# Kernel tuning notes

Hardware: AMD Instinct MI355X
Metric: run time of the kernel (lower is better)

Reference implementation:

```python
import jax, jax.numpy as jnp
import numpy as np

BS, NUM_PATCH, N_VARS, PATCH_LEN, D_MODEL = 32, 64, 321, 12, 128
TIME_RATIO, FREQ_RATIO = 0.5, 0.4


def setup_inputs() -> dict:
    key = jax.random.key(0)
    ks = jax.random.split(key, 7)
    x = jax.random.normal(ks[0], (BS, NUM_PATCH, N_VARS, PATCH_LEN), jnp.float32)
    W_in = jax.random.normal(ks[1], (PATCH_LEN, D_MODEL), jnp.float32) / np.sqrt(PATCH_LEN)
    b_in = jnp.zeros((D_MODEL,), jnp.float32)
    W_out = jax.random.normal(ks[2], (D_MODEL, PATCH_LEN), jnp.float32) / np.sqrt(D_MODEL)
    b_out = jnp.zeros((PATCH_LEN,), jnp.float32)
    # nn.Parameter(torch.zeros(1,1,1)) in the original; use small random scalars so grads are non-trivial
    time_mask_token = jax.random.normal(ks[3], (), jnp.float32) * 0.02
    freq_mask_token = jax.random.normal(ks[4], (), jnp.float32) * 0.02
    return {"x": x, "W_in": W_in, "b_in": b_in, "W_out": W_out, "b_out": b_out,
            "time_mask_token": time_mask_token, "freq_mask_token": freq_mask_token}


def _scatter_mask(idx, num_patch):
    # idx: [bs, n_vars, k] patch indices to mask (set False). Returns bool [bs, num_patch, n_vars].
    bs, nv, k = idx.shape
    m = jnp.ones((bs, num_patch, nv), dtype=bool)
    b = jnp.arange(bs)[:, None, None]
    v = jnp.arange(nv)[None, :, None]
    return m.at[b, idx, v].set(False)


def reference(x, W_in, b_in, W_out, b_out, time_mask_token, freq_mask_token):
    bs, num_patch, n_vars, patch_len = x.shape

    # patch2emb applied per token (equivalent to the gather-encode path since the
    # projection is pointwise per patch): [bs, np, nv, d_model]
    emb = jnp.einsum('bpvl,ld->bpvd', x, W_in) + b_in

    # ---- time masking: mask patches with highest coefficient of variation ----
    cv = jnp.std(x, axis=-1, ddof=1) / (jnp.mean(x, axis=-1) + 1e-6)  # [bs, np, nv]
    k_t = int(num_patch * TIME_RATIO)
    _, idx_t = jax.lax.top_k(jnp.transpose(cv, (0, 2, 1)), k_t)       # [bs, nv, k_t]
    mask_t = _scatter_mask(idx_t, num_patch)                           # True = keep
    tokens_t = jnp.where(mask_t[..., None], emb, time_mask_token)
    out_t = jnp.einsum('bpvd,dl->bpvl', tokens_t, W_out) + b_out

    # ---- freq masking: mask patches with lowest mean FFT magnitude ----
    mag = jnp.abs(jnp.fft.rfft(x, axis=-1))                            # [bs, np, nv, pl//2+1]
    score = mag.mean(axis=-1)                                          # [bs, np, nv]
    k_f = int(num_patch * FREQ_RATIO)
    _, idx_f = jax.lax.top_k(-jnp.transpose(score, (0, 2, 1)), k_f)    # smallest scores
    mask_f = _scatter_mask(idx_f, num_patch)
    tokens_f = jnp.where(mask_f[..., None], emb, freq_mask_token)
    out_f = jnp.einsum('bpvd,dl->bpvl', tokens_f, W_out) + b_out

    return out_t * 0.5 + out_f * 0.5
```

## Files before the change

### kernel.cpp

```cpp
#include <hip/hip_runtime.h>
#include <math.h>

constexpr int BS = 32, NP = 64, NV = 321, PL = 12, DM = 128;
constexpr int KT = 32;
constexpr int KF = 25;

__global__ void prep_kernel(const float* __restrict__ W_in,
                            const float* __restrict__ b_in,
                            const float* __restrict__ W_out,
                            const float* __restrict__ tt,
                            const float* __restrict__ ft,
                            float* __restrict__ prep) {
  int t = threadIdx.x;
  if (t < 144) {
    int i = t / 12, l = t % 12;
    float s = 0.f;
    for (int d = 0; d < DM; ++d) s += W_in[i * DM + d] * W_out[d * PL + l];
    prep[t] = s;
  } else if (t < 156) {
    int l = t - 144;
    float cs = 0.f, cb = 0.f;
    for (int d = 0; d < DM; ++d) {
      float w = W_out[d * PL + l];
      cs += w;
      cb += b_in[d] * w;
    }
    prep[144 + l] = cb;
    prep[156 + l] = tt[0] * cs;
    prep[168 + l] = ft[0] * cs;
  }
}

__global__ __launch_bounds__(256) void score_mask_kernel(
    const float* __restrict__ x,
    unsigned long long* __restrict__ mT,
    unsigned long long* __restrict__ mF) {
  const int wave = threadIdx.x >> 6;
  const int p = threadIdx.x & 63;
  const int bv = blockIdx.x * 4 + wave;
  const int b = bv / NV, v = bv % NV;

  const float4* xp = (const float4*)(x + ((size_t)(b * NP + p) * NV + v) * PL);
  float4 a0 = xp[0], a1 = xp[1], a2 = xp[2];
  float xv[12] = {a0.x, a0.y, a0.z, a0.w, a1.x, a1.y, a1.z, a1.w,
                  a2.x, a2.y, a2.z, a2.w};

  float s = 0.f;
#pragma unroll
  for (int i = 0; i < 12; ++i) s += xv[i];
  float m = s * (1.0f / 12.0f);
  float ss = 0.f;
#pragma unroll
  for (int i = 0; i < 12; ++i) {
    float d = xv[i] - m;
    ss += d * d;
  }
  float cv = sqrtf(ss * (1.0f / 11.0f)) / (m + 1e-6f);

  const float C30[12] = {1.f, 0.86602540378443864676f, 0.5f, 0.f,
                         -0.5f, -0.86602540378443864676f, -1.f,
                         -0.86602540378443864676f, -0.5f, 0.f,
                         0.5f, 0.86602540378443864676f};
  const float S30[12] = {0.f, 0.5f, 0.86602540378443864676f, 1.f,
                         0.86602540378443864676f, 0.5f, 0.f,
                         -0.5f, -0.86602540378443864676f, -1.f,
                         -0.86602540378443864676f, -0.5f};
  float acc = 0.f;
#pragma unroll
  for (int k = 0; k < 7; ++k) {
    float re = 0.f, im = 0.f;
#pragma unroll
    for (int n = 0; n < 12; ++n) {
      int idx = (k * n) % 12;
      re += xv[n] * C30[idx];
      im += xv[n] * S30[idx];
    }
    acc += sqrtf(re * re + im * im);
  }
  float fs = acc * (1.0f / 7.0f);

  __shared__ float scv[4][64];
  __shared__ float sfs[4][64];
  scv[wave][p] = cv;
  sfs[wave][p] = fs;
  __syncthreads();
  int rt = 0, rf = 0;
#pragma unroll 4
  for (int q = 0; q < 64; ++q) {
    float cq = scv[wave][q];
    rt += (cq > cv || (cq == cv && q < p)) ? 1 : 0;
    float fq = sfs[wave][q];
    rf += (fq < fs || (fq == fs && q < p)) ? 1 : 0;
  }
  bool keep_t = (rt >= KT);
  bool keep_f = (rf >= KF);
  unsigned long long bt = __ballot(keep_t);
  unsigned long long bf = __ballot(keep_f);
  if (p == 0) {
    mT[bv] = bt;
    mF[bv] = bf;
  }
}

__global__ __launch_bounds__(256) void decode_kernel(
    const float* __restrict__ x,
    const float* __restrict__ b_out,
    const float* __restrict__ prep,
    const unsigned long long* __restrict__ mT,
    const unsigned long long* __restrict__ mF,
    float* __restrict__ out) {
  const int bp = blockIdx.x;
  const int b = bp >> 6, p = bp & 63;
  __shared__ float sM[144], sc[12], sSt[12], sSf[12], sb[12];
  __shared__ float xs[NV * PL];
  const int tid = threadIdx.x;
  if (tid < 144) sM[tid] = prep[tid];
  else if (tid < 156) sc[tid - 144] = prep[tid];
  else if (tid < 168) sSt[tid - 156] = prep[tid];
  else if (tid < 180) sSf[tid - 168] = prep[tid];
  else if (tid < 192) sb[tid - 180] = b_out[tid - 180];

  const float4* xbp = (const float4*)(x + (size_t)bp * (NV * PL));
  float4* xs4 = (float4*)xs;
  for (int i = tid; i < NV * PL / 4; i += 256) xs4[i] = xbp[i];
  __syncthreads();

  float* outp = out + (size_t)bp * (NV * PL);
  for (int e = tid; e < NV * PL; e += 256) {
    int v = e / 12, l = e - v * 12;
    float E = sc[l];
#pragma unroll
    for (int i = 0; i < 12; ++i) E += xs[v * 12 + i] * sM[i * 12 + l];
    unsigned long long mt = mT[b * NV + v];
    unsigned long long mf = mF[b * NV + v];
    bool kt = (mt >> p) & 1ull;
    bool kf = (mf >> p) & 1ull;
    float at = kt ? E : sSt[l];
    float af = kf ? E : sSf[l];
    outp[e] = 0.5f * (at + af) + sb[l];
  }
}

extern "C" void kernel_launch(void* const* d_in, const int* in_sizes, int n_in,
                              void* d_out, int out_size, void* d_ws,
                              size_t ws_size, hipStream_t stream) {
  const float* x = (const float*)d_in[0];
  const float* W_in = (const float*)d_in[1];
  const float* b_in = (const float*)d_in[2];
  const float* W_out = (const float*)d_in[3];
  const float* b_out = (const float*)d_in[4];
  const float* tt = (const float*)d_in[5];
  const float* ft = (const float*)d_in[6];
  float* out = (float*)d_out;

  float* prep = (float*)d_ws;
  unsigned long long* mT = (unsigned long long*)((char*)d_ws + 1024);
  unsigned long long* mF = mT + BS * NV;

  hipLaunchKernelGGL(prep_kernel, dim3(1), dim3(192), 0, stream, W_in, b_in,
                     W_out, tt, ft, prep);
  hipLaunchKernelGGL(score_mask_kernel, dim3(BS * NV / 4), dim3(256), 0,
                     stream, x, mT, mF);
  hipLaunchKernelGGL(decode_kernel, dim3(BS * NP), dim3(256), 0, stream, x,
                     b_out, prep, mT, mF, out);
}
```

Baseline: 129.1 us.

## Fuse prep, scoring/masking and decode into one kernel with ballot-based top-k

Replaces three launches with a single fused kernel. Each block loads an 8-variable strip of x for all 64 patches into padded shared memory, recomputes the small weight product per block, scores patches and builds the masks, then decodes and writes float4 outputs. The O(64) rank loop is replaced by a wave-wide radix select over ordered float bits using ballots, and the 12-point DFT uses a symmetric closed form. This removes the second read of x and the launch overhead, at the cost of recomputing W_in·W_out in every block and using strided x loads.

```diff
diff --git a/kernel.cpp b/kernel.cpp
--- a/kernel.cpp
+++ b/kernel.cpp
@@ -4,140 +4,214 @@
 constexpr int BS = 32, NP = 64, NV = 321, PL = 12, DM = 128;
 constexpr int KT = 32;
 constexpr int KF = 25;
-
-__global__ void prep_kernel(const float* __restrict__ W_in,
-                            const float* __restrict__ b_in,
-                            const float* __restrict__ W_out,
-                            const float* __restrict__ tt,
-                            const float* __restrict__ ft,
-                            float* __restrict__ prep) {
-  int t = threadIdx.x;
+constexpr int VB = 8;
+constexpr int NCHUNK = (NV + VB - 1) / VB;
+constexpr int RSTRIDE = 64 * 13 + 4;
+
+__device__ __forceinline__ unsigned ord(float f) {
+  unsigned u = __float_as_uint(f);
+  return ((int)u < 0) ? ~u : (u | 0x80000000u);
+}
+
+__device__ __forceinline__ bool keep_not_topk(unsigned u, int K, int lane) {
+  unsigned thr = 0;
+#pragma unroll
+  for (int bit = 31; bit >= 0; --bit) {
+    unsigned cand = thr | (1u << bit);
+    unsigned long long b = __ballot(u >= cand);
+    if (__popcll(b) >= K) thr = cand;
+  }
+  int cnt_gt = __popcll(__ballot(u > thr));
+  unsigned long long eq = __ballot(u == thr);
+  int r_eq = __popcll(eq & ((1ull << lane) - 1ull));
+  bool masked = (u > thr) || ((u == thr) && (r_eq < (K - cnt_gt)));
+  return !masked;
+}
+
+__global__ __launch_bounds__(256) void fused_kernel(
+    const float* __restrict__ x, const float* __restrict__ W_in,
+    const float* __restrict__ b_in, const float* __restrict__ W_out,
+    const float* __restrict__ b_out, const float* __restrict__ tt,
+    const float* __restrict__ ft, float* __restrict__ out) {
+  __shared__ float xs[VB * RSTRIDE];
+  __shared__ float sM[144];
+  __shared__ float sc[12], sSt[12], sSf[12], sb[12];
+  __shared__ unsigned long long smT[VB], smF[VB];
+
+  const int t = threadIdx.x;
+  const int blk = blockIdx.x;
+  const int b = blk / NCHUNK;
+  const int chunk = blk - b * NCHUNK;
+  const int v0 = chunk * VB;
+  const int nv = min(VB, NV - v0);
+
+  const float* xb = x + (size_t)(b * 64) * (NV * PL) + v0 * PL;
+  const int nf4 = 64 * nv * 3;
+  float4 st[6];
+  int soff[6];
+  int cnt = 0;
+  for (int j = t; j < nf4; j += 256) {
+    int p = j / (nv * 3);
+    int r = j - p * (nv * 3);
+    int vv = r / 3;
+    int l0 = (r - vv * 3) * 4;
+    st[cnt] = *(const float4*)(xb + (size_t)p * (NV * PL) + vv * PL + l0);
+    soff[cnt] = vv * RSTRIDE + p * 13 + l0;
+    ++cnt;
+  }
+
   if (t < 144) {
-    int i = t / 12, l = t % 12;
-    float s = 0.f;
-    for (int d = 0; d < DM; ++d) s += W_in[i * DM + d] * W_out[d * PL + l];
-    prep[t] = s;
-  } else if (t < 156) {
-    int l = t - 144;
+    const int i = t / 12, l = t - (t / 12) * 12;
+    const float4* Wi = (const float4*)(W_in + i * DM);
+    float acc = 0.f;
+#pragma unroll 8
+    for (int d4 = 0; d4 < 32; ++d4) {
+      float4 a = Wi[d4];
+      const float* wo = W_out + d4 * 48 + l;
+      acc += a.x * wo[0];
+      acc += a.y * wo[12];
+      acc += a.z * wo[24];
+      acc += a.w * wo[36];
+    }
+    sM[t] = acc;
+  } else if (t < 168) {
+    const int l = (t - 144) % 12;
     float cs = 0.f, cb = 0.f;
+#pragma unroll 8
     for (int d = 0; d < DM; ++d) {
-      float w = W_out[d * PL + l];
+      float w = W_out[d * 12 + l];
       cs += w;
       cb += b_in[d] * w;
     }
-    prep[144 + l] = cb;
-    prep[156 + l] = tt[0] * cs;
-    prep[168 + l] = ft[0] * cs;
-  }
-}
-
-__global__ __launch_bounds__(256) void score_mask_kernel(
-    const float* __restrict__ x,
-    unsigned long long* __restrict__ mT,
-    unsigned long long* __restrict__ mF) {
-  const int wave = threadIdx.x >> 6;
-  const int p = threadIdx.x & 63;
-  const int bv = blockIdx.x * 4 + wave;
-  const int b = bv / NV, v = bv % NV;
-
-  const float4* xp = (const float4*)(x + ((size_t)(b * NP + p) * NV + v) * PL);
-  float4 a0 = xp[0], a1 = xp[1], a2 = xp[2];
-  float xv[12] = {a0.x, a0.y, a0.z, a0.w, a1.x, a1.y, a1.z, a1.w,
-                  a2.x, a2.y, a2.z, a2.w};
-
-  float s = 0.f;
-#pragma unroll
-  for (int i = 0; i < 12; ++i) s += xv[i];
-  float m = s * (1.0f / 12.0f);
-  float ss = 0.f;
+    if (t < 156) {
+      sc[l] = cb;
+      sSt[l] = tt[0] * cs;
+    } else {
+      sSf[l] = ft[0] * cs;
+    }
+  } else if (t < 180) {
+    sb[t - 168] = b_out[t - 168];
+  }
+
+  for (int q = 0; q < cnt; ++q) {
+    float* d = xs + soff[q];
+    d[0] = st[q].x;
+    d[1] = st[q].y;
+    d[2] = st[q].z;
+    d[3] = st[q].w;
+  }
+  __syncthreads();
+
+  const int wv = t >> 6, lane = t & 63;
+  const float H = 0.86602540378443864676f;
+#pragma unroll
+  for (int k = 0; k < 2; ++k) {
+    const int vv = wv * 2 + k;
+    if (vv < nv) {
+      const float* xp = xs + vv * RSTRIDE + lane * 13;
+      float xv[12];
+#pragma unroll
+      for (int i = 0; i < 12; ++i) xv[i] = xp[i];
+
+      float s = 0.f;
+#pragma unroll
+      for (int i = 0; i < 12; ++i) s += xv[i];
+      const float m = s * (1.0f / 12.0f);
+      float ss = 0.f;
+#pragma unroll
+      for (int i = 0; i < 12; ++i) {
+        float d = xv[i] - m;
+        ss += d * d;
+      }
+      const float cv = sqrtf(ss * (1.0f / 11.0f)) / (m + 1e-6f);
+
+      const float e1 = xv[1] + xv[11], e2 = xv[2] + xv[10],
+                  e3 = xv[3] + xv[9], e4 = xv[4] + xv[8], e5 = xv[5] + xv[7];
+      const float o1 = xv[1] - xv[11], o2 = xv[2] - xv[10],
+                  o3 = xv[3] - xv[9], o4 = xv[4] - xv[8], o5 = xv[5] - xv[7];
+      float mag = fabsf(xv[0] + xv[6] + e1 + e2 + e3 + e4 + e5);
+      float re = xv[0] - xv[6] + H * (e1 - e5) + 0.5f * (e2 - e4);
+      float im = 0.5f * (o1 + o5) + H * (o2 + o4) + o3;
+      mag += sqrtf(re * re + im * im);
+      re = xv[0] + xv[6] + 0.5f * (e1 + e5) - 0.5f * (e2 + e4) - e3;
+      im = H * (o1 + o2 - o4 - o5);
+      mag += sqrtf(re * re + im * im);
+      re = xv[0] - xv[6] - e2 + e4;
+      im = o1 - o3 + o5;
+      mag += sqrtf(re * re + im * im);
+      re = xv[0] + xv[6] - 0.5f * (e1 + e2 + e4 + e5) + e3;
+      im = H * (o1 - o2 + o4 - o5);
+      mag += sqrtf(re * re + im * im);
+      re = xv[0] - xv[6] + H * (e5 - e1) + 0.5f * (e2 - e4);
+      im = 0.5f * (o1 + o5) - H * (o2 + o4) + o3;
+      mag += sqrtf(re * re + im * im);
+      re = xv[0] + xv[6] - e1 + e2 - e3 + e4 - e5;
+      mag += fabsf(re);
+      const float fs = mag * (1.0f / 7.0f);
+
+      const bool kt = keep_not_topk(ord(cv), KT, lane);
+      const bool kf = keep_not_topk(~ord(fs), KF, lane);
+      unsigned long long bt = __ballot(kt), bf = __ballot(kf);
+      if (lane == 0) {
+        smT[vv] = bt;
+        smF[vv] = bf;
+      }
+    }
+  }
+  __syncthreads();
+
+  const int p2 = t >> 2;
+  const int vv0 = (t & 3) * 2;
+  float xv2[2][12], E[2][12];
+  const bool val0 = vv0 < nv, val1 = (vv0 + 1) < nv;
+#pragma unroll
+  for (int j = 0; j < 2; ++j) {
+    const float* xp = xs + (vv0 + j) * RSTRIDE + p2 * 13;
+#pragma unroll
+    for (int i = 0; i < 12; ++i) xv2[j][i] = xp[i];
+  }
+#pragma unroll
+  for (int l = 0; l < 12; ++l) {
+    E[0][l] = sc[l];
+    E[1][l] = sc[l];
+  }
+  const float4* M4 = (const float4*)sM;
 #pragma unroll
   for (int i = 0; i < 12; ++i) {
-    float d = xv[i] - m;
-    ss += d * d;
-  }
-  float cv = sqrtf(ss * (1.0f / 11.0f)) / (m + 1e-6f);
-
-  const float C30[12] = {1.f, 0.86602540378443864676f, 0.5f, 0.f,
-                         -0.5f, -0.86602540378443864676f, -1.f,
-                         -0.86602540378443864676f, -0.5f, 0.f,
-                         0.5f, 0.86602540378443864676f};
-  const float S30[12] = {0.f, 0.5f, 0.86602540378443864676f, 1.f,
-                         0.86602540378443864676f, 0.5f, 0.f,
-                         -0.5f, -0.86602540378443864676f, -1.f,
-                         -0.86602540378443864676f, -0.5f};
-  float acc = 0.f;
-#pragma unroll
-  for (int k = 0; k < 7; ++k) {
-    float re = 0.f, im = 0.f;
-#pragma unroll
-    for (int n = 0; n < 12; ++n) {
-      int idx = (k * n) % 12;
-      re += xv[n] * C30[idx];
-      im += xv[n] * S30[idx];
-    }
-    acc += sqrtf(re * re + im * im);
-  }
-  float fs = acc * (1.0f / 7.0f);
-
-  __shared__ float scv[4][64];
-  __shared__ float sfs[4][64];
-  scv[wave][p] = cv;
-  sfs[wave][p] = fs;
-  __syncthreads();
-  int rt = 0, rf = 0;
-#pragma unroll 4
-  for (int q = 0; q < 64; ++q) {
-    float cq = scv[wave][q];
-    rt += (cq > cv || (cq == cv && q < p)) ? 1 : 0;
-    float fq = sfs[wave][q];
-    rf += (fq < fs || (fq == fs && q < p)) ? 1 : 0;
-  }
-  bool keep_t = (rt >= KT);
-  bool keep_f = (rf >= KF);
-  unsigned long long bt = __ballot(keep_t);
-  unsigned long long bf = __ballot(keep_f);
-  if (p == 0) {
-    mT[bv] = bt;
-    mF[bv] = bf;
-  }
-}
-
-__global__ __launch_bounds__(256) void decode_kernel(
-    const float* __restrict__ x,
-    const float* __restrict__ b_out,
-    const float* __restrict__ prep,
-    const unsigned long long* __restrict__ mT,
-    const unsigned long long* __restrict__ mF,
-    float* __restrict__ out) {
-  const int bp = blockIdx.x;
-  const int b = bp >> 6, p = bp & 63;
-  __shared__ float sM[144], sc[12], sSt[12], sSf[12], sb[12];
-  __shared__ float xs[NV * PL];
-  const int tid = threadIdx.x;
-  if (tid < 144) sM[tid] = prep[tid];
-  else if (tid < 156) sc[tid - 144] = prep[tid];
-  else if (tid < 168) sSt[tid - 156] = prep[tid];
-  else if (tid < 180) sSf[tid - 168] = prep[tid];
-  else if (tid < 192) sb[tid - 180] = b_out[tid - 180];
-
-  const float4* xbp = (const float4*)(x + (size_t)bp * (NV * PL));
-  float4* xs4 = (float4*)xs;
-  for (int i = tid; i < NV * PL / 4; i += 256) xs4[i] = xbp[i];
-  __syncthreads();
-
-  float* outp = out + (size_t)bp * (NV * PL);
-  for (int e = tid; e < NV * PL; e += 256) {
-    int v = e / 12, l = e - v * 12;
-    float E = sc[l];
-#pragma unroll
-    for (int i = 0; i < 12; ++i) E += xs[v * 12 + i] * sM[i * 12 + l];
-    unsigned long long mt = mT[b * NV + v];
-    unsigned long long mf = mF[b * NV + v];
-    bool kt = (mt >> p) & 1ull;
-    bool kf = (mf >> p) & 1ull;
-    float at = kt ? E : sSt[l];
-    float af = kf ? E : sSf[l];
-    outp[e] = 0.5f * (at + af) + sb[l];
+    float4 m0 = M4[i * 3], m1 = M4[i * 3 + 1], m2 = M4[i * 3 + 2];
+    float a0 = xv2[0][i], a1 = xv2[1][i];
+    E[0][0] += a0 * m0.x;  E[0][1] += a0 * m0.y;
+    E[0][2] += a0 * m0.z;  E[0][3] += a0 * m0.w;
+    E[0][4] += a0 * m1.x;  E[0][5] += a0 * m1.y;
+    E[0][6] += a0 * m1.z;  E[0][7] += a0 * m1.w;
+    E[0][8] += a0 * m2.x;  E[0][9] += a0 * m2.y;
+    E[0][10] += a0 * m2.z; E[0][11] += a0 * m2.w;
+    E[1][0] += a1 * m0.x;  E[1][1] += a1 * m0.y;
+    E[1][2] += a1 * m0.z;  E[1][3] += a1 * m0.w;
+    E[1][4] += a1 * m1.x;  E[1][5] += a1 * m1.y;
+    E[1][6] += a1 * m1.z;  E[1][7] += a1 * m1.w;
+    E[1][8] += a1 * m2.x;  E[1][9] += a1 * m2.y;
+    E[1][10] += a1 * m2.z; E[1][11] += a1 * m2.w;
+  }
+#pragma unroll
+  for (int j = 0; j < 2; ++j) {
+    if (j == 0 ? val0 : val1) {
+      const int vv = vv0 + j;
+      const bool kt = (smT[vv] >> p2) & 1ull;
+      const bool kf = (smF[vv] >> p2) & 1ull;
+      float o[12];
+#pragma unroll
+      for (int l = 0; l < 12; ++l) {
+        float e = E[j][l];
+        float at = kt ? e : sSt[l];
+        float af = kf ? e : sSf[l];
+        o[l] = 0.5f * (at + af) + sb[l];
+      }
+      float* op = out + ((size_t)(b * 64 + p2) * NV + v0 + vv) * PL;
+      ((float4*)op)[0] = make_float4(o[0], o[1], o[2], o[3]);
+      ((float4*)op)[1] = make_float4(o[4], o[5], o[6], o[7]);
+      ((float4*)op)[2] = make_float4(o[8], o[9], o[10], o[11]);
+    }
   }
 }
 
@@ -153,14 +227,6 @@
   const float* ft = (const float*)d_in[6];
   float* out = (float*)d_out;
 
-  float* prep = (float*)d_ws;
-  unsigned long long* mT = (unsigned long long*)((char*)d_ws + 1024);
-  unsigned long long* mF = mT + BS * NV;
-
-  hipLaunchKernelGGL(prep_kernel, dim3(1), dim3(192), 0, stream, W_in, b_in,
-                     W_out, tt, ft, prep);
-  hipLaunchKernelGGL(score_mask_kernel, dim3(BS * NV / 4), dim3(256), 0,
-                     stream, x, mT, mF);
-  hipLaunchKernelGGL(decode_kernel, dim3(BS * NP), dim3(256), 0, stream, x,
-                     b_out, prep, mT, mF, out);
-}
+  hipLaunchKernelGGL(fused_kernel, dim3(BS * NCHUNK), dim3(256), 0, stream, x,
+                     W_in, b_in, W_out, b_out, tt, ft, out);
+}
```

Result: slower. 147.5 us (+14.2%).
